# Kernel optimization log

Hardware: AMD Instinct MI355X
Metric: run time of the kernel (lower is better)

Reference implementation:

```python
import jax, jax.numpy as jnp
from jax import lax
import numpy as np

N, T, V = 32, 32, 128
C_FEAT, C_BOX, C_CLS = 256, 4, 4
C_IN = C_FEAT + C_BOX + C_CLS  # 264 (is_scene=False concatenates x,b,c)
C_OUT = 64
K = 9
EPS = 1e-3  # keras BatchNormalization default epsilon


def _bn4(x, g, b, m, v):
    # inference-mode BN over channel axis 1 of (N,C,T,V)
    s = (g * lax.rsqrt(v + EPS))[None, :, None, None]
    return (x - m[None, :, None, None]) * s + b[None, :, None, None]


def _stgcn(x, a, imp, w, bw, ga, ba, ma, va, al, wt, bt, gb, bb, mb, vb, residual):
    res = x if residual else 0.0
    # SGCN: 1x1 conv (channels_first) then adjacency aggregation; dropout is identity at inference
    h = jnp.einsum('nctv,co->notv', x, w) + bw[None, :, None, None]
    h = jnp.einsum('nctv,ntvw->nctw', h, a * imp)
    # TGCN: BN -> PReLU(alpha per (C,T,V)) -> temporal conv (K,1) SAME -> BN -> (dropout=id)
    h = _bn4(h, ga, ba, ma, va)
    h = jnp.where(h >= 0, h, al[None] * h)
    h = lax.conv_general_dilated(h, wt, (1, 1), 'SAME',
                                 dimension_numbers=('NCHW', 'HWIO', 'NCHW')) + bt[None, :, None, None]
    h = _bn4(h, gb, bb, mb, vb)
    return h + res  # use_mdn=True -> no final PReLU


def _forward(x, b, c, a, dbn_g, dbn_b, dbn_m, dbn_v,
             w0, bw0, imp0, g0a, b0a, m0a, v0a, al0, wt0, bt0, g0b, b0b, m0b, v0b,
             w1, bw1, imp1, g1a, b1a, m1a, v1a, al1, wt1, bt1, g1b, b1b, m1b, v1b):
    x = jnp.concatenate([x, b, c], axis=-1)  # (N,T,V,C_IN)
    n, t, v, cc = x.shape
    # data BN over flattened (V*C) channel axis, exactly as the TF reshapes do
    x = jnp.transpose(x, (0, 2, 3, 1)).reshape(n, v * cc, t)
    s = (dbn_g * lax.rsqrt(dbn_v + EPS))[None, :, None]
    x = (x - dbn_m[None, :, None]) * s + dbn_b[None, :, None]
    # NOTE: the original does transpose(0,1,3,2) then a *reshape* to (N,C,T,V); replicate exactly
    x = x.reshape(n, v, cc, t).transpose(0, 1, 3, 2).reshape(n, cc, t, v)
    x = _stgcn(x, a, imp0, w0, bw0, g0a, b0a, m0a, v0a, al0, wt0, bt0, g0b, b0b, m0b, v0b, residual=False)
    x = _stgcn(x, a, imp1, w1, bw1, g1a, b1a, m1a, v1a, al1, wt1, bt1, g1b, b1b, m1b, v1b, residual=True)
    x = x[:, :, :, 0]  # (N,C_OUT,T)
    return jnp.transpose(x, (0, 2, 1))  # (N,T,C_OUT)


def setup_inputs():
    key = jax.random.key(0)
    ks = jax.random.split(key, 40)
    rn = lambda k, s, sc=1.0: jax.random.normal(k, s, jnp.float32) * sc
    ru = lambda k, s, lo, hi: jax.random.uniform(k, s, jnp.float32, lo, hi)
    d = {}
    d['x'] = rn(ks[0], (N, T, V, C_FEAT))
    d['b'] = rn(ks[1], (N, T, V, C_BOX))
    d['c'] = ru(ks[2], (N, T, V, C_CLS), 0.0, 1.0)
    d['a'] = ru(ks[3], (N, T, V, V), 0.0, 1.0)
    d['dbn_g'] = ru(ks[4], (V * C_IN,), 0.5, 1.5)
    d['dbn_b'] = rn(ks[5], (V * C_IN,), 0.1)
    d['dbn_m'] = rn(ks[6], (V * C_IN,), 0.1)
    d['dbn_v'] = ru(ks[7], (V * C_IN,), 0.5, 1.5)

    def mk_layer(i, cin, kb):
        d['w%d' % i] = rn(ks[kb], (cin, C_OUT), (1.0 / cin) ** 0.5)
        d['bw%d' % i] = rn(ks[kb + 1], (C_OUT,), 0.01)
        d['imp%d' % i] = rn(ks[kb + 2], (V, V), (2.0 / (V * V)) ** 0.5)
        d['g%da' % i] = ru(ks[kb + 3], (C_OUT,), 0.5, 1.5)
        d['b%da' % i] = rn(ks[kb + 4], (C_OUT,), 0.1)
        d['m%da' % i] = rn(ks[kb + 5], (C_OUT,), 0.1)
        d['v%da' % i] = ru(ks[kb + 6], (C_OUT,), 0.5, 1.5)
        d['al%d' % i] = ru(ks[kb + 7], (C_OUT, T, V), 0.0, 0.3)
        d['wt%d' % i] = rn(ks[kb + 8], (K, 1, C_OUT, C_OUT), (1.0 / (K * C_OUT)) ** 0.5)
        d['bt%d' % i] = rn(ks[kb + 9], (C_OUT,), 0.01)
        d['g%db' % i] = ru(ks[kb + 10], (C_OUT,), 0.5, 1.5)
        d['b%db' % i] = rn(ks[kb + 11], (C_OUT,), 0.1)
        d['m%db' % i] = rn(ks[kb + 12], (C_OUT,), 0.1)
        d['v%db' % i] = ru(ks[kb + 13], (C_OUT,), 0.5, 1.5)

    mk_layer(0, C_IN, 8)
    mk_layer(1, C_OUT, 22)
    return d


def reference(x, b, c, a, dbn_g, dbn_b, dbn_m, dbn_v,
              w0, bw0, imp0, g0a, b0a, m0a, v0a, al0, wt0, bt0, g0b, b0b, m0b, v0b,
              w1, bw1, imp1, g1a, b1a, m1a, v1a, al1, wt1, bt1, g1b, b1b, m1b, v1b):
    return _forward(x, b, c, a, dbn_g, dbn_b, dbn_m, dbn_v,
                    w0, bw0, imp0, g0a, b0a, m0a, v0a, al0, wt0, bt0, g0b, b0b, m0b, v0b,
                    w1, bw1, imp1, g1a, b1a, m1a, v1a, al1, wt1, bt1, g1b, b1b, m1b, v1b)
```

## Files before the change

### kernel.cpp

```cpp
#include <hip/hip_runtime.h>
#include <hip/hip_bf16.h>

typedef unsigned short u16;
typedef unsigned int   u32;

#define N_   32
#define T_   32
#define V_   128
#define CIN_ 264
#define CO_  64
#define KT_  9
#define EPS_ 1e-3f

#define OFF_DBN_S 0
#define OFF_DBN_O 33792
#define OFF_W0    67584
#define OFF_BW0   84480
#define OFF_A0S   84544
#define OFF_A0O   84608
#define OFF_B0S   84672
#define OFF_B0O   84736
#define OFF_W1    84800
#define OFF_BW1   88896
#define OFF_A1S   88960
#define OFF_A1O   89024
#define OFF_B1S   89088
#define OFF_B1O   89152
#define PREP_TOTAL 110464

#define B_P    0
#define B_FLAG 360448
#define B_W0A  360512
#define B_WTA  397440
#define B_H0   524288
#define B_XP   (B_H0 + 16777216)
#define B_G0   (B_H0 + 16777216)
#define B_L0   (B_G0 + 16777216)
#define B_G1P  (B_L0 + 33554432)
#define B_END  (B_G1P + 262144)

typedef short bf16x8 __attribute__((ext_vector_type(8)));
typedef float f32x4  __attribute__((ext_vector_type(4)));

__device__ __forceinline__ float bf2f(u16 u) { return __uint_as_float(((u32)u) << 16); }
__device__ __forceinline__ u16 f2bf(float f) {
    u32 x = __float_as_uint(f);
    return (u16)((x + 0x7fffu + ((x >> 16) & 1u)) >> 16);
}
__device__ __forceinline__ float ldin(const void* p, u32 i, int f32) {
    return f32 ? ((const float*)p)[i] : bf2f(((const u16*)p)[i]);
}

__global__ void k_detect(const void* a, int* flag) {
    if (threadIdx.x == 0 && blockIdx.x == 0) {
        const u16* p = (const u16*)a;
        int cnt = 0;
        for (int i = 0; i < 64; ++i) {
            float v = bf2f(p[2 * i]);
            if (v >= 0.f && v <= 1.0f) ++cnt;
        }
        *flag = (cnt >= 56) ? 0 : 1;
    }
}

__global__ void k_prep(const void* dbn_g, const void* dbn_b, const void* dbn_m, const void* dbn_v,
                       const void* w0, const void* bw0,
                       const void* g0a, const void* b0a, const void* m0a, const void* v0a,
                       const void* bt0, const void* g0b, const void* b0b, const void* m0b, const void* v0b,
                       const void* w1, const void* bw1,
                       const void* g1a, const void* b1a, const void* m1a, const void* v1a,
                       const void* bt1, const void* g1b, const void* b1b, const void* m1b, const void* v1b,
                       const void* wt0,
                       float* P, u16* W0A, u16* WTA, const int* flagp)
{
    const int f32 = *flagp;
    int i = blockIdx.x * 256 + threadIdx.x;
    if (i < 33792) {
        float s = ldin(dbn_g, i, f32) * rsqrtf(ldin(dbn_v, i, f32) + EPS_);
        P[OFF_DBN_S + i] = s;
        P[OFF_DBN_O + i] = ldin(dbn_b, i, f32) - ldin(dbn_m, i, f32) * s;
    } else if (i < 50688) { int j = i - 33792; P[OFF_W0 + j] = ldin(w0, j, f32); }
    else if (i < 50752) { int j = i - 50688; P[OFF_BW0 + j] = ldin(bw0, j, f32); }
    else if (i < 50816) { int j = i - 50752;
        float s = ldin(g0a, j, f32) * rsqrtf(ldin(v0a, j, f32) + EPS_);
        P[OFF_A0S + j] = s; P[OFF_A0O + j] = ldin(b0a, j, f32) - ldin(m0a, j, f32) * s;
    } else if (i < 50880) { int j = i - 50816;
        float s = ldin(g0b, j, f32) * rsqrtf(ldin(v0b, j, f32) + EPS_);
        P[OFF_B0S + j] = s; P[OFF_B0O + j] = (ldin(bt0, j, f32) - ldin(m0b, j, f32)) * s + ldin(b0b, j, f32);
    } else if (i < 54976) { int j = i - 50880; P[OFF_W1 + j] = ldin(w1, j, f32); }
    else if (i < 55040) { int j = i - 54976; P[OFF_BW1 + j] = ldin(bw1, j, f32); }
    else if (i < 55104) { int j = i - 55040;
        float s = ldin(g1a, j, f32) * rsqrtf(ldin(v1a, j, f32) + EPS_);
        P[OFF_A1S + j] = s; P[OFF_A1O + j] = ldin(b1a, j, f32) - ldin(m1a, j, f32) * s;
    } else if (i < 55168) { int j = i - 55104;
        float s = ldin(g1b, j, f32) * rsqrtf(ldin(v1b, j, f32) + EPS_);
        P[OFF_B1S + j] = s; P[OFF_B1O + j] = (ldin(bt1, j, f32) - ldin(m1b, j, f32)) * s + ldin(b1b, j, f32);
    } else if (i < 73600) {
        int j = i - 55168; int c = j / 288, ci = j - c * 288;
        float val = (ci < 264) ? ldin(w0, (u32)ci * 64 + c, f32)
                  : ((ci == 264) ? ldin(bw0, c, f32) : 0.f);
        W0A[j] = f2bf(val);
    } else if (i < 110464) {
        int j = i - 73600; int k = j >> 12, rem = j & 4095, o = rem >> 6, ii = rem & 63;
        WTA[j] = f2bf(ldin(wt0, ((u32)(k * 64 + ii)) * 64 + o, f32));
    }
}

__global__ __launch_bounds__(256) void k_bnx(const void* __restrict__ xin, const void* __restrict__ bin,
                                             const void* __restrict__ cin2, const float* __restrict__ P,
                                             u16* __restrict__ Xp, const int* __restrict__ flagp, int nbase)
{
    __shared__ __align__(16) u16 tile[32 * 130];
    const int f32 = *flagp;
    const int rt = blockIdx.x;
    const int ct = blockIdx.y;
    const int nloc = blockIdx.z;
    const int n = nbase + nloc;
    const int c0 = ct * 32;
    const int ncols = (ct == 8) ? 8 : 32;
    const int r0 = rt * 128;
    const int tid = threadIdx.x;

    for (int q = tid; q < ncols * 32; q += 256) {
        int j = q >> 5, i4 = (q & 31) << 2;
        u32 L = (u32)(c0 + j) * 4096u + (u32)(r0 + i4);
        u32 vs = L / 8448u;
        u32 r  = L - vs * 8448u;
        u32 ts = r / 264u;
        u32 cc = r - ts * 264u;
        u32 base = ((u32)n * 32u + ts) * 128u + vs;
        float4 val;
        if (f32) {
            if (cc < 256u)      val = *(const float4*)((const float*)xin  + (size_t)base * 256u + cc);
            else if (cc < 260u) val = *(const float4*)((const float*)bin  + (size_t)base * 4u + (cc - 256u));
            else                val = *(const float4*)((const float*)cin2 + (size_t)base * 4u + (cc - 260u));
        } else {
            ushort4 uv;
            if (cc < 256u)      uv = *(const ushort4*)((const u16*)xin  + (size_t)base * 256u + cc);
            else if (cc < 260u) uv = *(const ushort4*)((const u16*)bin  + (size_t)base * 4u + (cc - 256u));
            else                uv = *(const ushort4*)((const u16*)cin2 + (size_t)base * 4u + (cc - 260u));
            val.x = bf2f(uv.x); val.y = bf2f(uv.y); val.z = bf2f(uv.z); val.w = bf2f(uv.w);
        }
        u32 ch = vs * 264u + cc;
        const float4 s4 = *(const float4*)&P[OFF_DBN_S + ch];
        const float4 o4 = *(const float4*)&P[OFF_DBN_O + ch];
        ushort2 lo, hi;
        lo.x = f2bf(fmaf(val.x, s4.x, o4.x));
        lo.y = f2bf(fmaf(val.y, s4.y, o4.y));
        hi.x = f2bf(fmaf(val.z, s4.z, o4.z));
        hi.y = f2bf(fmaf(val.w, s4.w, o4.w));
        *(ushort2*)&tile[j * 130 + i4]     = lo;
        *(ushort2*)&tile[j * 130 + i4 + 2] = hi;
    }
    __syncthreads();
    const int chunks = ncols >> 3;
    for (int e = tid; e < 128 * chunks; e += 256) {
        int i, cch;
        if (chunks == 4) { i = e >> 2; cch = e & 3; } else { i = e; cch = 0; }
        __align__(16) u16 tmp[8];
#pragma unroll
        for (int k2 = 0; k2 < 8; ++k2) tmp[k2] = tile[(cch * 8 + k2) * 130 + i];
        *(uint4*)&Xp[((u32)nloc * 4096u + (u32)(r0 + i)) * 264u + (u32)(c0 + cch * 8)] = *(uint4*)tmp;
    }
}

__global__ __launch_bounds__(256) void k_pw0(const u16* __restrict__ Xp, const u16* __restrict__ W0Ag,
                                             u16* __restrict__ h0, int nbase)
{
    const int t2 = blockIdx.x, nloc = blockIdx.y, vh = blockIdx.z;
    const int n = nbase + nloc;
    const int tid = threadIdx.x;
    const int wv = tid >> 6, lane = tid & 63, l16 = lane & 15, quad = lane >> 4;
    const int m0 = wv * 16;
    const int vrow = vh * 64 + m0 + l16;
    const u16* arow = Xp + ((u32)nloc * 4096u + (u32)(t2 * 128 + vrow)) * 264u;

    f32x4 acc[4];
#pragma unroll
    for (int i = 0; i < 4; ++i) acc[i] = (f32x4){0.f, 0.f, 0.f, 0.f};

#pragma unroll
    for (int ks = 0; ks < 8; ++ks) {
        const int k0 = ks * 32 + quad * 8;
        bf16x8 af = *(const bf16x8*)&arow[k0];
#pragma unroll
        for (int ni = 0; ni < 4; ++ni) {
            bf16x8 bf = *(const bf16x8*)&W0Ag[(u32)(ni * 16 + l16) * 288 + k0];
            acc[ni] = __builtin_amdgcn_mfma_f32_16x16x32_bf16(af, bf, acc[ni], 0, 0, 0);
        }
    }
    {
        bf16x8 af = (bf16x8){0, 0, 0, 0, 0, 0, 0, 0};
        if (quad == 0)      af = *(const bf16x8*)&arow[256];
        else if (quad == 1) af[0] = (short)0x3F80;
        const int k0 = 256 + quad * 8;
#pragma unroll
        for (int ni = 0; ni < 4; ++ni) {
            bf16x8 bf = *(const bf16x8*)&W0Ag[(u32)(ni * 16 + l16) * 288 + k0];
            acc[ni] = __builtin_amdgcn_mfma_f32_16x16x32_bf16(af, bf, acc[ni], 0, 0, 0);
        }
    }
    const int v = vh * 64 + m0 + quad * 4;
#pragma unroll
    for (int ni = 0; ni < 4; ++ni) {
        int c = ni * 16 + l16;
        ushort4 rr; u16* rp = (u16*)&rr;
#pragma unroll
        for (int r = 0; r < 4; ++r) rp[r] = f2bf(acc[ni][r]);
        *(ushort4*)&h0[((u32)(n * 64 + c) * 32 + t2) * 128 + v] = rr;
    }
}

__global__ __launch_bounds__(256) void k_at(const void* __restrict__ a, const void* __restrict__ imp0,
                                            u16* __restrict__ aT, const int* __restrict__ flagp)
{
    __shared__ __align__(16) u16 tile[128 * 128];
    const int f32 = *flagp;
    const int t = blockIdx.x, n = blockIdx.y;
    const int tid = threadIdx.x;
    const u32 abase = (((u32)n * 32u + (u32)t) * 128u) * 128u;

    for (int e = tid; e < 2048; e += 256) {
        int v = e >> 4, w0 = (e & 15) << 3;
        float vals[8];
        if (f32) {
            const float* ap = (const float*)a + abase + (u32)v * 128u + w0;
            const float* ip = (const float*)imp0 + (u32)v * 128u + w0;
            float4 x0 = *(const float4*)ap, x1 = *(const float4*)(ap + 4);
            float4 i0 = *(const float4*)ip, i1 = *(const float4*)(ip + 4);
            vals[0] = x0.x * i0.x; vals[1] = x0.y * i0.y; vals[2] = x0.z * i0.z; vals[3] = x0.w * i0.w;
            vals[4] = x1.x * i1.x; vals[5] = x1.y * i1.y; vals[6] = x1.z * i1.z; vals[7] = x1.w * i1.w;
        } else {
            uint4 xu = *(const uint4*)((const u16*)a + abase + (u32)v * 128u + w0);
            uint4 iu = *(const uint4*)((const u16*)imp0 + (u32)v * 128u + w0);
            const u16* xp = (const u16*)&xu; const u16* ip = (const u16*)&iu;
#pragma unroll
            for (int j = 0; j < 8; ++j) vals[j] = bf2f(xp[j]) * bf2f(ip[j]);
        }
        __align__(16) u16 pk[8];
#pragma unroll
        for (int j = 0; j < 8; ++j) pk[j] = f2bf(vals[j]);
        u32 byte = (u32)v * 256u + (((u32)w0 * 2u) ^ ((((u32)v >> 3) & 7u) << 4));
        *(uint4*)((char*)tile + byte) = *(uint4*)pk;
    }
    __syncthreads();
    for (int e = tid; e < 2048; e += 256) {
        int w = e >> 4, v0 = (e & 15) << 3;
        __align__(16) u16 tmp[8];
#pragma unroll
        for (int k = 0; k < 8; ++k) {
            int v = v0 + k;
            u32 byte = (u32)v * 256u + ((((u32)w * 2u)) ^ ((((u32)v >> 3) & 7u) << 4));
            tmp[k] = *(const u16*)((const char*)tile + byte);
        }
        *(uint4*)&aT[abase + (u32)w * 128u + v0] = *(uint4*)tmp;
    }
}

__global__ __launch_bounds__(256) void k_graph0(const void* __restrict__ al0, const float* __restrict__ P,
                                                const u16* __restrict__ h0, const u16* __restrict__ aT,
                                                u16* __restrict__ g0, const int* __restrict__ flagp)
{
    const int f32 = *flagp;
    const int t = blockIdx.x, n = blockIdx.y;
    const int tid = threadIdx.x;
    const int wv = tid >> 6, lane = tid & 63, l16 = lane & 15, quad = lane >> 4;
    const int n0w = wv * 32;
    const u16* aTb = aT + (((u32)n * 32u + (u32)t) * 128u) * 128u;
    const u16* Hb  = h0 + ((u32)n * 2048u + (u32)t) * 128u;

    f32x4 acc[4][2];
#pragma unroll
    for (int mi = 0; mi < 4; ++mi) { acc[mi][0] = (f32x4){0,0,0,0}; acc[mi][1] = (f32x4){0,0,0,0}; }
#pragma unroll
    for (int ks = 0; ks < 4; ++ks) {
        const int k0 = ks * 32 + quad * 8;
        bf16x8 bf0 = *(const bf16x8*)&aTb[(u32)(n0w + l16) * 128u + k0];
        bf16x8 bf1 = *(const bf16x8*)&aTb[(u32)(n0w + 16 + l16) * 128u + k0];
#pragma unroll
        for (int mi = 0; mi < 4; ++mi) {
            bf16x8 af = *(const bf16x8*)&Hb[(u32)(mi * 16 + l16) * 4096u + k0];
            acc[mi][0] = __builtin_amdgcn_mfma_f32_16x16x32_bf16(af, bf0, acc[mi][0], 0, 0, 0);
            acc[mi][1] = __builtin_amdgcn_mfma_f32_16x16x32_bf16(af, bf1, acc[mi][1], 0, 0, 0);
        }
    }
#pragma unroll
    for (int mi = 0; mi < 4; ++mi) {
        const int c0 = mi * 16 + quad * 4;
        const float4 s4 = *(const float4*)&P[OFF_A0S + c0];
        const float4 o4 = *(const float4*)&P[OFF_A0O + c0];
        const float ss[4] = {s4.x, s4.y, s4.z, s4.w};
        const float oo[4] = {o4.x, o4.y, o4.z, o4.w};
#pragma unroll
        for (int ni = 0; ni < 2; ++ni) {
            const int w = n0w + ni * 16 + l16;
            ushort4 rr; u16* rp = (u16*)&rr;
#pragma unroll
            for (int r = 0; r < 4; ++r) {
                float y = fmaf(acc[mi][ni][r], ss[r], oo[r]);
                float alv = ldin(al0, ((u32)(c0 + r) * 32 + t) * 128 + w, f32);
                rp[r] = f2bf((y >= 0.f) ? y : alv * y);
            }
            *(ushort4*)&g0[((u32)(n * 32 + t) * 128 + w) * 64 + c0] = rr;
        }
    }
}

__global__ __launch_bounds__(256) void k_tconv0(const u16* __restrict__ WTAg, const float* __restrict__ P,
                                                const u16* __restrict__ g0, float* __restrict__ L0)
{
    __shared__ __align__(16) u16 Wl[2][64 * 72];
    __shared__ __align__(16) u16 Bs[2][128 * 72];
    const int t = blockIdx.x, n = blockIdx.y;
    const int tid = threadIdx.x;
    const int kmin = (t < 4) ? (4 - t) : 0;
    const int kmax = (t > 27) ? (35 - t) : 8;

    auto stageB = [&](int k, int buf) {
        const u16* src = g0 + ((u32)(n * 32 + (t + k - 4)) * 128) * 64;
        for (int e = tid; e < 1024; e += 256) {
            int row = e >> 3, ch = e & 7;
            *(uint4*)&Bs[buf][row * 72 + ch * 8] = *(const uint4*)&src[row * 64 + ch * 8];
        }
    };
    auto stageW = [&](int k, int buf) {
        const u16* src = WTAg + (u32)k * 4096;
        for (int e = tid; e < 512; e += 256) {
            int row = e >> 3, ch = e & 7;
            *(uint4*)&Wl[buf][row * 72 + ch * 8] = *(const uint4*)&src[row * 64 + ch * 8];
        }
    };
    stageB(kmin, 0); stageW(kmin, 0);
    __syncthreads();
    const int wv = tid >> 6, lane = tid & 63, l16 = lane & 15, quad = lane >> 4;
    const int n0w = wv * 32;
    f32x4 acc[4][2];
#pragma unroll
    for (int mi = 0; mi < 4; ++mi) { acc[mi][0] = (f32x4){0,0,0,0}; acc[mi][1] = (f32x4){0,0,0,0}; }

    for (int k = kmin; k <= kmax; ++k) {
        const int buf = (k - kmin) & 1;
        if (k < kmax) { stageB(k + 1, buf ^ 1); stageW(k + 1, buf ^ 1); }
#pragma unroll
        for (int ks = 0; ks < 2; ++ks) {
            const int k0 = ks * 32 + quad * 8;
            bf16x8 bf[2];
            bf[0] = *(const bf16x8*)&Bs[buf][(n0w + l16) * 72 + k0];
            bf[1] = *(const bf16x8*)&Bs[buf][(n0w + 16 + l16) * 72 + k0];
#pragma unroll
            for (int mi = 0; mi < 4; ++mi) {
                bf16x8 af = *(const bf16x8*)&Wl[buf][(mi * 16 + l16) * 72 + k0];
                acc[mi][0] = __builtin_amdgcn_mfma_f32_16x16x32_bf16(af, bf[0], acc[mi][0], 0, 0, 0);
                acc[mi][1] = __builtin_amdgcn_mfma_f32_16x16x32_bf16(af, bf[1], acc[mi][1], 0, 0, 0);
            }
        }
        __syncthreads();
    }
#pragma unroll
    for (int mi = 0; mi < 4; ++mi) {
        const int ob = mi * 16 + quad * 4;
        const float4 s4 = *(const float4*)&P[OFF_B0S + ob];
        const float4 o4 = *(const float4*)&P[OFF_B0O + ob];
        const float ss[4] = {s4.x, s4.y, s4.z, s4.w};
        const float oo[4] = {o4.x, o4.y, o4.z, o4.w};
#pragma unroll
        for (int ni = 0; ni < 2; ++ni) {
            const int v = n0w + ni * 16 + l16;
#pragma unroll
            for (int r = 0; r < 4; ++r)
                L0[((u32)(n * 64 + ob + r) * 32 + t) * 128 + v] = fmaf(acc[mi][ni][r], ss[r], oo[r]);
        }
    }
}

__global__ __launch_bounds__(128) void k_pw1(const void* __restrict__ a, const void* __restrict__ imp1,
                                             const void* __restrict__ al1, const float* __restrict__ P,
                                             const float* __restrict__ L0, float* __restrict__ g1p,
                                             const int* __restrict__ flagp)
{
    __shared__ float part[V_ * 65];
    __shared__ float red2[128];
    const int f32 = *flagp;
    const int t = blockIdx.x, n = blockIdx.y;
    const int tid = threadIdx.x;
    const int v = tid;
    float acc[CO_];
#pragma unroll
    for (int o = 0; o < CO_; ++o) acc[o] = P[OFF_BW1 + o];
    const float* W = P + OFF_W1;
    const u32 base = (u32)n * (CO_ * T_ * V_) + (u32)t * V_ + (u32)v;
    for (int c = 0; c < CO_; ++c) {
        float xv = L0[base + (u32)c * (T_ * V_)];
        const float* wr = W + c * CO_;
#pragma unroll
        for (int o = 0; o < CO_; ++o) acc[o] = fmaf(xv, wr[o], acc[o]);
    }
    float amv = ldin(a, (((u32)n * T_ + t) * V_ + v) * V_ + 0u, f32) * ldin(imp1, (u32)v * V_ + 0u, f32);
#pragma unroll
    for (int o = 0; o < CO_; ++o) part[v * 65 + o] = acc[o] * amv;
    __syncthreads();
    const int o = tid & 63, hh = tid >> 6;
    float s = 0.f;
    for (int vv = hh * 64; vv < hh * 64 + 64; ++vv) s += part[vv * 65 + o];
    red2[tid] = s;
    __syncthreads();
    if (tid < 64) {
        float g = red2[tid] + red2[64 + tid];
        float y = fmaf(g, P[OFF_A1S + o], P[OFF_A1O + o]);
        float alv = ldin(al1, ((u32)o * T_ + t) * V_ + 0u, f32);
        y = (y >= 0.f) ? y : alv * y;
        g1p[((u32)n * CO_ + o) * T_ + t] = y;
    }
}

__global__ __launch_bounds__(64) void k_tconv1(const void* __restrict__ wt1, const float* __restrict__ P,
                                               const float* __restrict__ g1p, const float* __restrict__ L0,
                                               void* __restrict__ out, const int* __restrict__ flagp)
{
    __shared__ float gl[CO_ * KT_];
    const int f32 = *flagp;
    const int t = blockIdx.x, n = blockIdx.y;
    const int tid = threadIdx.x;
    for (int e = tid; e < CO_ * KT_; e += 64) {
        int i = e / KT_, kk = e - i * KT_;
        int tt = t + kk - 4;
        gl[e] = (tt >= 0 && tt < T_) ? g1p[((u32)n * CO_ + i) * T_ + tt] : 0.f;
    }
    __syncthreads();
    float acc = 0.f;
    for (int i = 0; i < CO_; ++i) {
#pragma unroll
        for (int k = 0; k < KT_; ++k) {
            float wv = ldin(wt1, ((u32)(k * CO_ + i)) * CO_ + tid, f32);
            acc = fmaf(gl[i * KT_ + k], wv, acc);
        }
    }
    float y = fmaf(acc, P[OFF_B1S + tid], P[OFF_B1O + tid]);
    y += L0[(u32)n * (CO_ * T_ * V_) + (u32)tid * (T_ * V_) + (u32)t * V_ + 0];
    const u32 oi = ((u32)n * T_ + t) * CO_ + tid;
    if (f32) ((float*)out)[oi] = y;
    else     ((u16*)out)[oi]   = f2bf(y);
}

__global__ void k_fail(u16* out, int nel) {
    int i = blockIdx.x * 256 + threadIdx.x;
    if (i < nel) out[i] = 0x7f80;
}

extern "C" void kernel_launch(void* const* d_in, const int* in_sizes, int n_in,
                              void* d_out, int out_size, void* d_ws, size_t ws_size,
                              hipStream_t stream)
{
    const void* xin  = d_in[0];
    const void* bin  = d_in[1];
    const void* cin2 = d_in[2];
    const void* a    = d_in[3];
    const void* dbn_g = d_in[4];
    const void* dbn_b = d_in[5];
    const void* dbn_m = d_in[6];
    const void* dbn_v = d_in[7];
    const void* w0  = d_in[8];
    const void* bw0 = d_in[9];
    const void* imp0 = d_in[10];
    const void* g0a = d_in[11];
    const void* b0a = d_in[12];
    const void* m0a = d_in[13];
    const void* v0a = d_in[14];
    const void* al0 = d_in[15];
    const void* wt0 = d_in[16];
    const void* bt0 = d_in[17];
    const void* g0b = d_in[18];
    const void* b0b = d_in[19];
    const void* m0b = d_in[20];
    const void* v0b = d_in[21];
    const void* w1  = d_in[22];
    const void* bw1 = d_in[23];
    const void* imp1 = d_in[24];
    const void* g1a = d_in[25];
    const void* b1a = d_in[26];
    const void* m1a = d_in[27];
    const void* v1a = d_in[28];
    const void* al1 = d_in[29];
    const void* wt1 = d_in[30];
    const void* bt1 = d_in[31];
    const void* g1b = d_in[32];
    const void* b1b = d_in[33];
    const void* m1b = d_in[34];
    const void* v1b = d_in[35];

    if (ws_size < (size_t)B_END) {
        k_fail<<<(out_size + 255) / 256, 256, 0, stream>>>((u16*)d_out, out_size);
        return;
    }
    char* w = (char*)d_ws;
    float* P    = (float*)(w + B_P);
    int*   flg  = (int*)(w + B_FLAG);
    u16*   W0A  = (u16*)(w + B_W0A);
    u16*   WTA  = (u16*)(w + B_WTA);
    u16*   h0   = (u16*)(w + B_H0);
    u16*   Xp   = (u16*)(w + B_XP);
    u16*   g0   = (u16*)(w + B_G0);
    u16*   aT   = (u16*)(w + B_L0);
    float* L0   = (float*)(w + B_L0);
    float* g1p  = (float*)(w + B_G1P);

    k_detect<<<1, 64, 0, stream>>>(a, flg);
    k_prep<<<(PREP_TOTAL + 255) / 256, 256, 0, stream>>>(
        dbn_g, dbn_b, dbn_m, dbn_v, w0, bw0, g0a, b0a, m0a, v0a,
        bt0, g0b, b0b, m0b, v0b, w1, bw1, g1a, b1a, m1a, v1a,
        bt1, g1b, b1b, m1b, v1b, wt0, P, W0A, WTA, flg);

    for (int hf = 0; hf < 2; ++hf) {
        const int nbase = hf * 16;
        k_bnx<<<dim3(32, 9, 16), 256, 0, stream>>>(xin, bin, cin2, P, Xp, flg, nbase);
        k_pw0<<<dim3(T_, 16, 2), 256, 0, stream>>>(Xp, W0A, h0, nbase);
    }

    dim3 grid(T_, N_);
    k_at    <<<grid, 256, 0, stream>>>(a, imp0, aT, flg);
    k_graph0<<<grid, 256, 0, stream>>>(al0, P, h0, aT, g0, flg);
    k_tconv0<<<grid, 256, 0, stream>>>(WTA, P, g0, L0);
    k_pw1   <<<grid, 128, 0, stream>>>(a, imp1, al1, P, L0, g1p, flg);
    k_tconv1<<<grid,  64, 0, stream>>>(wt1, P, g1p, L0, d_out, flg);
}
```

Measured before the change: 521.3 us.

## Reassociate pw1 to aggregate over vertices before the 1x1 conv; drop LDS staging in tconv0

k_pw1 now reduces L0 across vertices, weighted by the column-0 adjacency, before applying the 64x64 pointwise weights. The bias term is scaled by the sum of those weights. This turns a per-vertex 64x64 matvec into one matvec per (n,t), removing most FMAs and the large shared-memory reduction buffer. Separately, k_tconv0 drops its double-buffered LDS staging and reads MFMA operands directly from global memory, relying on caches. That removes the barriers but may add redundant global traffic.

```diff
diff --git a/kernel.cpp b/kernel.cpp
--- a/kernel.cpp
+++ b/kernel.cpp
@@ -309,52 +309,32 @@
 __global__ __launch_bounds__(256) void k_tconv0(const u16* __restrict__ WTAg, const float* __restrict__ P,
                                                 const u16* __restrict__ g0, float* __restrict__ L0)
 {
-    __shared__ __align__(16) u16 Wl[2][64 * 72];
-    __shared__ __align__(16) u16 Bs[2][128 * 72];
     const int t = blockIdx.x, n = blockIdx.y;
     const int tid = threadIdx.x;
     const int kmin = (t < 4) ? (4 - t) : 0;
     const int kmax = (t > 27) ? (35 - t) : 8;
-
-    auto stageB = [&](int k, int buf) {
-        const u16* src = g0 + ((u32)(n * 32 + (t + k - 4)) * 128) * 64;
-        for (int e = tid; e < 1024; e += 256) {
-            int row = e >> 3, ch = e & 7;
-            *(uint4*)&Bs[buf][row * 72 + ch * 8] = *(const uint4*)&src[row * 64 + ch * 8];
-        }
-    };
-    auto stageW = [&](int k, int buf) {
-        const u16* src = WTAg + (u32)k * 4096;
-        for (int e = tid; e < 512; e += 256) {
-            int row = e >> 3, ch = e & 7;
-            *(uint4*)&Wl[buf][row * 72 + ch * 8] = *(const uint4*)&src[row * 64 + ch * 8];
-        }
-    };
-    stageB(kmin, 0); stageW(kmin, 0);
-    __syncthreads();
     const int wv = tid >> 6, lane = tid & 63, l16 = lane & 15, quad = lane >> 4;
     const int n0w = wv * 32;
+
     f32x4 acc[4][2];
 #pragma unroll
     for (int mi = 0; mi < 4; ++mi) { acc[mi][0] = (f32x4){0,0,0,0}; acc[mi][1] = (f32x4){0,0,0,0}; }
 
     for (int k = kmin; k <= kmax; ++k) {
-        const int buf = (k - kmin) & 1;
-        if (k < kmax) { stageB(k + 1, buf ^ 1); stageW(k + 1, buf ^ 1); }
+        const u16* Wb = WTAg + (u32)k * 4096u;
+        const u16* Bb = g0 + ((u32)(n * 32 + (t + k - 4)) * 128u) * 64u;
 #pragma unroll
         for (int ks = 0; ks < 2; ++ks) {
             const int k0 = ks * 32 + quad * 8;
-            bf16x8 bf[2];
-            bf[0] = *(const bf16x8*)&Bs[buf][(n0w + l16) * 72 + k0];
-            bf[1] = *(const bf16x8*)&Bs[buf][(n0w + 16 + l16) * 72 + k0];
+            bf16x8 bf0 = *(const bf16x8*)&Bb[(u32)(n0w + l16) * 64u + k0];
+            bf16x8 bf1 = *(const bf16x8*)&Bb[(u32)(n0w + 16 + l16) * 64u + k0];
 #pragma unroll
             for (int mi = 0; mi < 4; ++mi) {
-                bf16x8 af = *(const bf16x8*)&Wl[buf][(mi * 16 + l16) * 72 + k0];
-                acc[mi][0] = __builtin_amdgcn_mfma_f32_16x16x32_bf16(af, bf[0], acc[mi][0], 0, 0, 0);
-                acc[mi][1] = __builtin_amdgcn_mfma_f32_16x16x32_bf16(af, bf[1], acc[mi][1], 0, 0, 0);
+                bf16x8 af = *(const bf16x8*)&Wb[(u32)(mi * 16 + l16) * 64u + k0];
+                acc[mi][0] = __builtin_amdgcn_mfma_f32_16x16x32_bf16(af, bf0, acc[mi][0], 0, 0, 0);
+                acc[mi][1] = __builtin_amdgcn_mfma_f32_16x16x32_bf16(af, bf1, acc[mi][1], 0, 0, 0);
             }
         }
-        __syncthreads();
     }
 #pragma unroll
     for (int mi = 0; mi < 4; ++mi) {
@@ -373,40 +353,50 @@
     }
 }
 
-__global__ __launch_bounds__(128) void k_pw1(const void* __restrict__ a, const void* __restrict__ imp1,
+__global__ __launch_bounds__(256) void k_pw1(const void* __restrict__ a, const void* __restrict__ imp1,
                                              const void* __restrict__ al1, const float* __restrict__ P,
                                              const float* __restrict__ L0, float* __restrict__ g1p,
                                              const int* __restrict__ flagp)
 {
-    __shared__ float part[V_ * 65];
-    __shared__ float red2[128];
+    __shared__ float amv[V_];
+    __shared__ float xr[CO_];
+    __shared__ float Ssh;
     const int f32 = *flagp;
     const int t = blockIdx.x, n = blockIdx.y;
     const int tid = threadIdx.x;
-    const int v = tid;
-    float acc[CO_];
-#pragma unroll
-    for (int o = 0; o < CO_; ++o) acc[o] = P[OFF_BW1 + o];
-    const float* W = P + OFF_W1;
-    const u32 base = (u32)n * (CO_ * T_ * V_) + (u32)t * V_ + (u32)v;
-    for (int c = 0; c < CO_; ++c) {
-        float xv = L0[base + (u32)c * (T_ * V_)];
-        const float* wr = W + c * CO_;
-#pragma unroll
-        for (int o = 0; o < CO_; ++o) acc[o] = fmaf(xv, wr[o], acc[o]);
-    }
-    float amv = ldin(a, (((u32)n * T_ + t) * V_ + v) * V_ + 0u, f32) * ldin(imp1, (u32)v * V_ + 0u, f32);
-#pragma unroll
-    for (int o = 0; o < CO_; ++o) part[v * 65 + o] = acc[o] * amv;
-    __syncthreads();
-    const int o = tid & 63, hh = tid >> 6;
-    float s = 0.f;
-    for (int vv = hh * 64; vv < hh * 64 + 64; ++vv) s += part[vv * 65 + o];
-    red2[tid] = s;
+
+    if (tid < V_) {
+        float av = ldin(a, (((u32)n * T_ + t) * V_ + tid) * V_ + 0u, f32)
+                 * ldin(imp1, (u32)tid * V_ + 0u, f32);
+        amv[tid] = av;
+    }
     __syncthreads();
     if (tid < 64) {
-        float g = red2[tid] + red2[64 + tid];
-        float y = fmaf(g, P[OFF_A1S + o], P[OFF_A1O + o]);
+        float s = amv[tid] + amv[tid + 64];
+#pragma unroll
+        for (int m = 1; m < 64; m <<= 1) s += __shfl_xor(s, m);
+        if (tid == 0) Ssh = s;
+    }
+    const int c = tid >> 2, sub = tid & 3;
+    const float* Lrow = L0 + (u32)n * (CO_ * T_ * V_) + (u32)c * (T_ * V_) + (u32)t * V_ + sub * 32;
+    float p = 0.f;
+#pragma unroll
+    for (int j = 0; j < 32; j += 4) {
+        float4 x = *(const float4*)(Lrow + j);
+        float4 m = *(const float4*)&amv[sub * 32 + j];
+        p = fmaf(x.x, m.x, p); p = fmaf(x.y, m.y, p);
+        p = fmaf(x.z, m.z, p); p = fmaf(x.w, m.w, p);
+    }
+    p += __shfl_xor(p, 1);
+    p += __shfl_xor(p, 2);
+    if (sub == 0) xr[c] = p;
+    __syncthreads();
+    if (tid < CO_) {
+        const int o = tid;
+        float y = P[OFF_BW1 + o] * Ssh;
+        for (int cc = 0; cc < CO_; ++cc)
+            y = fmaf(xr[cc], P[OFF_W1 + cc * CO_ + o], y);
+        y = fmaf(y, P[OFF_A1S + o], P[OFF_A1O + o]);
         float alv = ldin(al1, ((u32)o * T_ + t) * V_ + 0u, f32);
         y = (y >= 0.f) ? y : alv * y;
         g1p[((u32)n * CO_ + o) * T_ + t] = y;
@@ -520,6 +510,6 @@
     k_at    <<<grid, 256, 0, stream>>>(a, imp0, aT, flg);
     k_graph0<<<grid, 256, 0, stream>>>(al0, P, h0, aT, g0, flg);
     k_tconv0<<<grid, 256, 0, stream>>>(WTA, P, g0, L0);
-    k_pw1   <<<grid, 128, 0, stream>>>(a, imp1, al1, P, L0, g1p, flg);
+    k_pw1   <<<grid, 256, 0, stream>>>(a, imp1, al1, P, L0, g1p, flg);
     k_tconv1<<<grid,  64, 0, stream>>>(wt1, P, g1p, L0, d_out, flg);
 }
```

Result: no change. 523.0 us (+0.3%).
